# Optimization experiments

Hardware: AMD Instinct MI355X
Metric: run time of the kernel (lower is better)

Reference implementation:

```python
import jax, jax.numpy as jnp
import numpy as np

K = 2          # kernel_size
NQ = 4         # n_qubits = K*K
NL = 2         # n_layers


def setup_inputs() -> dict:
    key = jax.random.key(0)
    ks = jax.random.split(key, 6)
    x = jax.random.uniform(ks[0], (64, 1, 128, 128), jnp.float32, 0.0, np.pi)
    conv_w = jax.random.normal(ks[1], (1, 1, K, K), jnp.float32) * 0.5
    conv_b = jax.random.normal(ks[2], (1,), jnp.float32) * 0.1
    ry_angles = jax.random.normal(ks[3], (NL, NQ), jnp.float32)  # fixed RY params
    head_w = jax.random.normal(ks[4], (1, 2), jnp.float32) * 0.5
    head_b = jax.random.normal(ks[5], (1,), jnp.float32) * 0.1
    return {"x": x, "conv_w": conv_w, "conv_b": conv_b,
            "ry_angles": ry_angles, "head_w": head_w, "head_b": head_b}


def _rx(state, theta, wire):
    # state: (N, 2,2,2,2) complex; theta: (N,) batched angle
    ax = wire + 1
    st = jnp.moveaxis(state, ax, 1)
    s0, s1 = st[:, 0], st[:, 1]                      # (N, 2,2,2)
    c = jnp.cos(theta * 0.5).reshape((-1, 1, 1, 1))
    s = jnp.sin(theta * 0.5).reshape((-1, 1, 1, 1))
    n0 = c * s0 - 1j * s * s1
    n1 = -1j * s * s0 + c * s1
    return jnp.moveaxis(jnp.stack([n0, n1], axis=1), 1, ax)


def _ry(state, phi, wire):
    # phi: scalar shared angle
    ax = wire + 1
    st = jnp.moveaxis(state, ax, 1)
    s0, s1 = st[:, 0], st[:, 1]
    c = jnp.cos(phi * 0.5)
    s = jnp.sin(phi * 0.5)
    n0 = c * s0 - s * s1
    n1 = s * s0 + c * s1
    return jnp.moveaxis(jnp.stack([n0, n1], axis=1), 1, ax)


def _cnot(state, ctrl, tgt):
    ca, ta = ctrl + 1, tgt + 1
    st = jnp.moveaxis(state, (ca, ta), (1, 2))       # (N, 2, 2, rest)
    new = jnp.stack([st[:, 0], st[:, 1, ::-1]], axis=1)  # flip target where ctrl=1
    return jnp.moveaxis(new, (1, 2), (ca, ta))


def _quantum_expval_z0(patch_flat, ry_angles):
    # patch_flat: (N, 4) -> expval PauliZ(wire 0), shape (N,)
    N = patch_flat.shape[0]
    state = jnp.zeros((N, 2, 2, 2, 2), jnp.complex64).at[:, 0, 0, 0, 0].set(1.0)
    for w in range(NQ):
        state = _rx(state, patch_flat[:, w], w)
    for l in range(NL):
        for w in range(NQ):
            state = _ry(state, ry_angles[l, w], w)
        for w in range(0, NQ - 1, 2):
            state = _cnot(state, w, w + 1)
    p = jnp.real(state) ** 2 + jnp.imag(state) ** 2   # (N,2,2,2,2)
    return p[:, 0].sum(axis=(1, 2, 3)) - p[:, 1].sum(axis=(1, 2, 3))


def reference(x, conv_w, conv_b, ry_angles, head_w, head_b):
    B, _, H, W = x.shape
    # all KxK sliding patches, feature order (c, kh, kw) row-major == patch.view(-1)
    patches = jax.lax.conv_general_dilated_patches(x, (K, K), (1, 1), 'VALID')  # (B,4,Ph,Pw)
    Ph, Pw = patches.shape[2], patches.shape[3]
    pf = patches.transpose(0, 2, 3, 1).reshape(-1, K * K)   # (N, 4)
    conv_out = pf @ conv_w.reshape(K * K) + conv_b[0]       # (N,)
    q_out = _quantum_expval_z0(pf, ry_angles)               # (N,)
    per_patch = head_w[0, 0] * conv_out + head_w[0, 1] * q_out + head_b[0]
    out = per_patch.reshape(B, Ph * Pw).mean(axis=1)        # mean over windows
    return out[:, None]
```

## Files before the change

kernel.cpp:

```cpp
#include <hip/hip_runtime.h>
#include <math.h>


#define XW 128
#define NP (127 * 127)
#define NB 64
#define NBLK 16
#define BLK 256

__device__ __forceinline__ void circuit_coeffs(const float* __restrict__ ry,
                                               float k[5]) {
    float U[4][4] = {{1,0,0,0},{0,1,0,0},{0,0,1,0},{0,0,0,1}};
    for (int l = 0; l < 2; ++l) {
        float s0, c0, s1, c1;
        __sincosf(0.5f * ry[l*4+0], &s0, &c0);
        __sincosf(0.5f * ry[l*4+1], &s1, &c1);
        for (int q1 = 0; q1 < 2; ++q1)
            for (int c = 0; c < 4; ++c) {
                float a = U[q1][c], d = U[2+q1][c];
                U[q1][c]   = c0*a - s0*d;
                U[2+q1][c] = s0*a + c0*d;
            }
        for (int m = 0; m < 2; ++m)
            for (int c = 0; c < 4; ++c) {
                float a = U[2*m][c], d = U[2*m+1][c];
                U[2*m][c]   = c1*a - s1*d;
                U[2*m+1][c] = s1*a + c1*d;
            }
        for (int c = 0; c < 4; ++c) { float t = U[2][c]; U[2][c] = U[3][c]; U[3][c] = t; }
    }
    float pA=0, pB=0, pC=0, pD=0, pAD=0, pBC=0;
    for (int r = 0; r < 4; ++r) {
        float g = (r < 2) ? 1.f : -1.f;
        pA  += g * U[r][0] * U[r][0];
        pB  += g * U[r][1] * U[r][1];
        pC  += g * U[r][2] * U[r][2];
        pD  += g * U[r][3] * U[r][3];
        pAD += g * U[r][0] * U[r][3];
        pBC += g * U[r][1] * U[r][2];
    }
    k[0] = 0.25f * (pA + pB + pC + pD);
    k[1] = 0.25f * (pA + pB - pC - pD);
    k[2] = 0.25f * (pA - pB + pC - pD);
    k[3] = 0.25f * (pA - pB - pC + pD);
    k[4] = 0.50f * (pBC - pAD);
}

__global__ __launch_bounds__(BLK) void row_kernel(
    const float* __restrict__ x,
    const float* __restrict__ conv_w,
    const float* __restrict__ head_w,
    const float* __restrict__ ry,
    float* __restrict__ part)
{
    __shared__ float sk[4];
    __shared__ float red[BLK / 64];

    const int tid  = threadIdx.x;
    const int lane = tid & 63;
    const int wave = tid >> 6;
    const int half = lane >> 5;
    const int col0 = (lane & 31) << 2;
    const int img  = blockIdx.y;
    const int row  = (blockIdx.x << 3) + (wave << 1) + half;

    if (tid == 0) {
        float k[5];
        circuit_coeffs(ry, k);
        const float hw1 = head_w[1];
        sk[0] = hw1 * k[1]; sk[1] = hw1 * k[2];
        sk[2] = hw1 * k[3]; sk[3] = hw1 * k[4];
    }
    __syncthreads();

    const float hw0 = head_w[0];
    const float w0 = hw0 * conv_w[0], w1 = hw0 * conv_w[1];
    const float w2 = hw0 * conv_w[2], w3 = hw0 * conv_w[3];
    const float k1 = sk[0], k2 = sk[1], k3 = sk[2], k4 = sk[3];

    const float P = (row < 127 ? w0 : 0.f) + (row > 0 ? w2 : 0.f);
    const float Q = (row < 127 ? w1 : 0.f) + (row > 0 ? w3 : 0.f);
    const float PQ = P + Q;

    const float4 e = ((const float4*)(x + ((size_t)img * 128 + row) * XW))
                         [lane & 31];

    float acc = e.x * (col0 == 0 ? P : PQ)
              + e.y * PQ
              + e.z * PQ
              + e.w * (col0 == 124 ? Q : PQ);

    if (row < 127) {
        float s0,c0,s1,c1,s2,c2,s3,c3;
        __sincosf(e.x, &s0, &c0);
        __sincosf(e.y, &s1, &c1);
        __sincosf(e.z, &s2, &c2);
        __sincosf(e.w, &s3, &c3);
        const float cn = __shfl_down(c0, 1, 64);
        const float sn = __shfl_down(s0, 1, 64);
        acc += k1 * c0 + k2 * c1 + k3 * c0 * c1 + k4 * s0 * s1;
        acc += k1 * c1 + k2 * c2 + k3 * c1 * c2 + k4 * s1 * s2;
        acc += k1 * c2 + k2 * c3 + k3 * c2 * c3 + k4 * s2 * s3;
        if (col0 < 124)
            acc += k1 * c3 + k2 * cn + k3 * c3 * cn + k4 * s3 * sn;
    }

    for (int off = 32; off > 0; off >>= 1)
        acc += __shfl_down(acc, off, 64);
    if (lane == 0) red[wave] = acc;
    __syncthreads();
    if (tid == 0)
        part[img * NBLK + blockIdx.x] = red[0] + red[1] + red[2] + red[3];
}

__global__ __launch_bounds__(64) void final_kernel(
    const float* __restrict__ part,
    const float* __restrict__ conv_b,
    const float* __restrict__ ry,
    const float* __restrict__ head_w,
    const float* __restrict__ head_b,
    float* __restrict__ out)
{
    const int b = threadIdx.x;
    float k[5];
    circuit_coeffs(ry, k);
    float sum = 0.f;
    for (int s = 0; s < NBLK; ++s) sum += part[b * NBLK + s];
    const float cconst = head_w[0] * conv_b[0] + head_w[1] * k[0] + head_b[0];
    out[b] = sum * (1.0f / NP) + cconst;
}

extern "C" void kernel_launch(void* const* d_in, const int* in_sizes, int n_in,
                              void* d_out, int out_size, void* d_ws, size_t ws_size,
                              hipStream_t stream) {
    const float* x      = (const float*)d_in[0];
    const float* conv_w = (const float*)d_in[1];
    const float* conv_b = (const float*)d_in[2];
    const float* ry     = (const float*)d_in[3];
    const float* head_w = (const float*)d_in[4];
    const float* head_b = (const float*)d_in[5];
    float* out  = (float*)d_out;
    float* part = (float*)d_ws;

    dim3 grid(NBLK, NB);
    row_kernel<<<grid, BLK, 0, stream>>>(x, conv_w, head_w, ry, part);
    final_kernel<<<1, 64, 0, stream>>>(part, conv_b, ry, head_w, head_b, out);
}
```

Measured before the change: 67.35 us.

## Fuse row and final kernels into one block per image

Replaces the two-kernel scheme (16 blocks per image writing partials, then a single-block final reduction) with one 1024-thread block per image. Each thread handles four rows, hoists all four float4 loads and the sincos work ahead of the barrier, reduces in-block, and writes the output directly. This removes the second launch and the partial-sum round trip through global memory. In exchange the grid shrinks to 64 blocks, leaving many compute units idle.

```diff
diff --git a/kernel.cpp b/kernel.cpp
--- a/kernel.cpp
+++ b/kernel.cpp
@@ -5,8 +5,7 @@
 #define XW 128
 #define NP (127 * 127)
 #define NB 64
-#define NBLK 16
-#define BLK 256
+#define BLK 1024
 
 __device__ __forceinline__ void circuit_coeffs(const float* __restrict__ ry,
                                                float k[5]) {
@@ -46,23 +45,31 @@
     k[4] = 0.50f * (pBC - pAD);
 }
 
-__global__ __launch_bounds__(BLK) void row_kernel(
+__global__ __launch_bounds__(BLK) void fused_kernel(
     const float* __restrict__ x,
     const float* __restrict__ conv_w,
+    const float* __restrict__ conv_b,
+    const float* __restrict__ ry,
     const float* __restrict__ head_w,
-    const float* __restrict__ ry,
-    float* __restrict__ part)
+    const float* __restrict__ head_b,
+    float* __restrict__ out)
 {
-    __shared__ float sk[4];
+    __shared__ float sk[5];
     __shared__ float red[BLK / 64];
 
-    const int tid  = threadIdx.x;
-    const int lane = tid & 63;
-    const int wave = tid >> 6;
-    const int half = lane >> 5;
-    const int col0 = (lane & 31) << 2;
-    const int img  = blockIdx.y;
-    const int row  = (blockIdx.x << 3) + (wave << 1) + half;
+    const int tid   = threadIdx.x;
+    const int lane  = tid & 63;
+    const int wave  = tid >> 6;
+    const int half  = lane >> 5;
+    const int col0  = (lane & 31) << 2;
+    const int img   = blockIdx.x;
+    const int rbase = (wave << 1) + half;
+
+    const float4* xr = (const float4*)(x + (size_t)img * 128 * XW);
+    float4 ee[4];
+    #pragma unroll
+    for (int p = 0; p < 4; ++p)
+        ee[p] = xr[(rbase + (p << 5)) * 32 + (lane & 31)];
 
     if (tid == 0) {
         float k[5];
@@ -70,7 +77,20 @@
         const float hw1 = head_w[1];
         sk[0] = hw1 * k[1]; sk[1] = hw1 * k[2];
         sk[2] = hw1 * k[3]; sk[3] = hw1 * k[4];
+        sk[4] = head_w[0] * conv_b[0] + hw1 * k[0] + head_b[0];
     }
+
+    float cA[4][4], sA[4][4], cN[4], sN[4];
+    #pragma unroll
+    for (int p = 0; p < 4; ++p) {
+        __sincosf(ee[p].x, &sA[p][0], &cA[p][0]);
+        __sincosf(ee[p].y, &sA[p][1], &cA[p][1]);
+        __sincosf(ee[p].z, &sA[p][2], &cA[p][2]);
+        __sincosf(ee[p].w, &sA[p][3], &cA[p][3]);
+        cN[p] = __shfl_down(cA[p][0], 1, 64);
+        sN[p] = __shfl_down(sA[p][0], 1, 64);
+    }
+
     __syncthreads();
 
     const float hw0 = head_w[0];
@@ -78,56 +98,43 @@
     const float w2 = hw0 * conv_w[2], w3 = hw0 * conv_w[3];
     const float k1 = sk[0], k2 = sk[1], k3 = sk[2], k4 = sk[3];
 
-    const float P = (row < 127 ? w0 : 0.f) + (row > 0 ? w2 : 0.f);
-    const float Q = (row < 127 ? w1 : 0.f) + (row > 0 ? w3 : 0.f);
-    const float PQ = P + Q;
+    float acc = 0.f;
+    #pragma unroll
+    for (int p = 0; p < 4; ++p) {
+        const int row = rbase + (p << 5);
+        const float P  = (row < 127 ? w0 : 0.f) + (row > 0 ? w2 : 0.f);
+        const float Q  = (row < 127 ? w1 : 0.f) + (row > 0 ? w3 : 0.f);
+        const float PQ = P + Q;
 
-    const float4 e = ((const float4*)(x + ((size_t)img * 128 + row) * XW))
-                         [lane & 31];
+        acc += ee[p].x * (col0 == 0 ? P : PQ)
+             + ee[p].y * PQ
+             + ee[p].z * PQ
+             + ee[p].w * (col0 == 124 ? Q : PQ);
 
-    float acc = e.x * (col0 == 0 ? P : PQ)
-              + e.y * PQ
-              + e.z * PQ
-              + e.w * (col0 == 124 ? Q : PQ);
-
-    if (row < 127) {
-        float s0,c0,s1,c1,s2,c2,s3,c3;
-        __sincosf(e.x, &s0, &c0);
-        __sincosf(e.y, &s1, &c1);
-        __sincosf(e.z, &s2, &c2);
-        __sincosf(e.w, &s3, &c3);
-        const float cn = __shfl_down(c0, 1, 64);
-        const float sn = __shfl_down(s0, 1, 64);
-        acc += k1 * c0 + k2 * c1 + k3 * c0 * c1 + k4 * s0 * s1;
-        acc += k1 * c1 + k2 * c2 + k3 * c1 * c2 + k4 * s1 * s2;
-        acc += k1 * c2 + k2 * c3 + k3 * c2 * c3 + k4 * s2 * s3;
-        if (col0 < 124)
-            acc += k1 * c3 + k2 * cn + k3 * c3 * cn + k4 * s3 * sn;
+        if (row < 127) {
+            const float c0 = cA[p][0], c1 = cA[p][1];
+            const float c2 = cA[p][2], c3 = cA[p][3];
+            const float s0 = sA[p][0], s1 = sA[p][1];
+            const float s2 = sA[p][2], s3 = sA[p][3];
+            acc += k1 * c0 + k2 * c1 + k3 * c0 * c1 + k4 * s0 * s1;
+            acc += k1 * c1 + k2 * c2 + k3 * c1 * c2 + k4 * s1 * s2;
+            acc += k1 * c2 + k2 * c3 + k3 * c2 * c3 + k4 * s2 * s3;
+            if (col0 < 124)
+                acc += k1 * c3 + k2 * cN[p] + k3 * c3 * cN[p]
+                     + k4 * s3 * sN[p];
+        }
     }
 
     for (int off = 32; off > 0; off >>= 1)
         acc += __shfl_down(acc, off, 64);
     if (lane == 0) red[wave] = acc;
     __syncthreads();
-    if (tid == 0)
-        part[img * NBLK + blockIdx.x] = red[0] + red[1] + red[2] + red[3];
-}
-
-__global__ __launch_bounds__(64) void final_kernel(
-    const float* __restrict__ part,
-    const float* __restrict__ conv_b,
-    const float* __restrict__ ry,
-    const float* __restrict__ head_w,
-    const float* __restrict__ head_b,
-    float* __restrict__ out)
-{
-    const int b = threadIdx.x;
-    float k[5];
-    circuit_coeffs(ry, k);
-    float sum = 0.f;
-    for (int s = 0; s < NBLK; ++s) sum += part[b * NBLK + s];
-    const float cconst = head_w[0] * conv_b[0] + head_w[1] * k[0] + head_b[0];
-    out[b] = sum * (1.0f / NP) + cconst;
+    if (wave == 0) {
+        float v = (lane < BLK / 64) ? red[lane] : 0.f;
+        for (int off = 8; off > 0; off >>= 1)
+            v += __shfl_down(v, off, 64);
+        if (lane == 0) out[img] = v * (1.0f / NP) + sk[4];
+    }
 }
 
 extern "C" void kernel_launch(void* const* d_in, const int* in_sizes, int n_in,
@@ -139,10 +146,8 @@
     const float* ry     = (const float*)d_in[3];
     const float* head_w = (const float*)d_in[4];
     const float* head_b = (const float*)d_in[5];
-    float* out  = (float*)d_out;
-    float* part = (float*)d_ws;
+    float* out = (float*)d_out;
 
-    dim3 grid(NBLK, NB);
-    row_kernel<<<grid, BLK, 0, stream>>>(x, conv_w, head_w, ry, part);
-    final_kernel<<<1, 64, 0, stream>>>(part, conv_b, ry, head_w, head_b, out);
+    fused_kernel<<<dim3(NB), dim3(BLK), 0, stream>>>(
+        x, conv_w, conv_b, ry, head_w, head_b, out);
 }
```

Result: no change. 66.93 us (-0.6%).
